# Performance work log

Measured on AMD Instinct MI355X. Metric: run time of the kernel, lower is better.

Reference implementation:

```python
import jax, jax.numpy as jnp
import numpy as np

N_HEAD = 8
N_VIEWS = 26
C = 256
H = W = 32
B_SCENE = 2


def _get_default_angles():
    # Reconstructed: bottom pole, top pole, then 3 rings of 8 azimuths at elev 45/0/-45.
    angs = [(0.0, -90.0), (0.0, 90.0)]
    for phi in (45.0, 0.0, -45.0):
        for k in range(8):
            angs.append((45.0 * k, phi))
    return np.array(angs)


def _angle_select():
    a = _get_default_angles()
    d = np.abs(a.reshape(26, 1, 2) - a.reshape(1, 26, 2))
    d = np.sum(np.minimum(d, 360 - d), axis=2)
    ab = d == 45
    ab[0, -8::2] = True
    ab[-8::2, 0] = True
    ab[1, 2:10:2] = True
    ab[2:10:2, 1] = True
    return [np.argwhere(ab[i]).reshape(-1) for i in range(26)]


def _mha_index(i):
    return i if i < 2 else (i - 2) // 8 + 2


def _mha(q, kv, Wqkv, bqkv, Wo, bo):
    # torch nn.MultiheadAttention, batch_first: packed in_proj, scale = 1/sqrt(head_dim)
    c = q.shape[-1]
    D = c // N_HEAD
    Wq, Wk, Wv = Wqkv[:c], Wqkv[c:2 * c], Wqkv[2 * c:]
    bq, bk, bv = bqkv[:c], bqkv[c:2 * c], bqkv[2 * c:]
    qp = q @ Wq.T + bq
    kp = kv @ Wk.T + bk
    vp = kv @ Wv.T + bv
    B, S, _ = qp.shape
    K = kp.shape[1]
    qh = qp.reshape(B, S, N_HEAD, D).transpose(0, 2, 1, 3)
    kh = kp.reshape(B, K, N_HEAD, D).transpose(0, 2, 1, 3)
    vh = vp.reshape(B, K, N_HEAD, D).transpose(0, 2, 1, 3)
    scores = jnp.einsum('bhqd,bhkd->bhqk', qh, kh) / jnp.sqrt(jnp.asarray(D, qh.dtype))
    att = jax.nn.softmax(scores, axis=-1)
    o = jnp.einsum('bhqk,bhkd->bhqd', att, vh).transpose(0, 2, 1, 3).reshape(B, S, c)
    return o @ Wo.T + bo


def setup_inputs() -> dict:
    key = jax.random.key(0)
    k1, k2, k3 = jax.random.split(key, 3)
    scale = 1.0 / np.sqrt(C)
    return {
        'x': jax.random.normal(k1, (B_SCENE * N_VIEWS, C, H, W), dtype=jnp.float32),
        'w_qkv': jax.random.normal(k2, (5, 3 * C, C), dtype=jnp.float32) * scale,
        'b_qkv': jnp.zeros((5, 3 * C), dtype=jnp.float32),
        'w_out': jax.random.normal(k3, (5, C, C), dtype=jnp.float32) * scale,
        'b_out': jnp.zeros((5, C), dtype=jnp.float32),
    }


def reference(x, w_qkv, b_qkv, w_out, b_out):
    bt, c, h, w = x.shape
    B = bt // N_VIEWS
    # (b t) c h w -> b t (h w) c
    xr = x.reshape(B, N_VIEWS, c, h * w).transpose(0, 1, 3, 2)
    sel = _angle_select()
    outs = []
    for i in range(N_VIEWS):
        m = _mha_index(i)
        q = xr[:, i]                                  # [B, S, c]
        kv = xr[:, sel[i]].reshape(B, -1, c)          # [B, n_nbr*S, c]
        outs.append(_mha(q, kv, w_qkv[m], b_qkv[m], w_out[m], b_out[m]))
    y = jnp.stack(outs, axis=1)                       # b t s c
    return y.transpose(0, 1, 3, 2).reshape(bt, c, h, w)
```

## Files before the change

### kernel.cpp

```cpp
#include <hip/hip_runtime.h>
#include <hip/hip_bf16.h>

#define NV 26
#define NS 1024
#define NC 256
#define NH 8
#define ND 32
#define NPAIR 66

typedef unsigned short u16;
typedef unsigned int u32;
typedef short short8_t __attribute__((ext_vector_type(8)));
typedef float f32x4 __attribute__((ext_vector_type(4)));
typedef unsigned int u32x4 __attribute__((ext_vector_type(4)));

__constant__ int c_view_m[NV]  = {0,1,2,2,2,2,2,2,2,2,3,3,3,3,3,3,3,3,4,4,4,4,4,4,4,4};
__constant__ int c_view_nk[NV] = {4,4,4,3,4,3,4,3,4,3,4,4,4,4,4,4,4,4,4,3,4,3,4,3,4,3};
__constant__ int c_view_kv[NV][4] = {
  {0,1,2,3},      {4,5,6,7},      {8,10,16,17},   {9,11,18,-1},
  {8,10,12,19},   {11,13,20,-1},  {8,12,14,21},   {13,15,22,-1},
  {8,14,16,23},   {9,15,24,-1},   {25,34,40,41},  {26,33,35,42},
  {27,34,36,43},  {28,35,37,44},  {29,36,38,45},  {30,37,39,46},
  {31,38,40,47},  {32,33,39,48},  {49,50,59,65},  {51,58,60,-1},
  {49,52,59,61},  {53,60,62,-1},  {49,54,61,63},  {55,62,64,-1},
  {49,56,63,65},  {57,58,64,-1}
};
__constant__ int c_pair_m[NPAIR] = {
  0,0,0,0, 1,1,1,1,
  2,2,2,2,2,2,2,2,2,2,2,2,2,2,2,2,2,
  3,3,3,3,3,3,3,3,3,3,3,3,3,3,3,3,3,3,3,3,3,3,3,3,
  4,4,4,4,4,4,4,4,4,4,4,4,4,4,4,4,4
};
__constant__ int c_pair_j[NPAIR] = {
  18,20,22,24, 2,4,6,8,
  1,2,3,4,5,6,7,8,9,10,11,12,13,14,15,16,17,
  2,3,4,5,6,7,8,9,10,11,12,13,14,15,16,17,18,19,20,21,22,23,24,25,
  0,10,11,12,13,14,15,16,17,18,19,20,21,22,23,24,25
};

__device__ __forceinline__ float bf16_to_f32(u16 u) {
  return __uint_as_float(((u32)u) << 16);
}
__device__ __forceinline__ u16 f32_to_bf16(float f) {
  u32 u = __float_as_uint(f);
  u32 r = (u + 0x7fffu + ((u >> 16) & 1u)) >> 16;
  return (u16)r;
}
__device__ __forceinline__ float ld_src(const void* p, size_t i, bool isf) {
  return isf ? ((const float*)p)[i] : bf16_to_f32(((const u16*)p)[i]);
}
__device__ __forceinline__ u32 pack_bf16x2_rne(float a, float b) {
  __hip_bfloat162 h = __float22bfloat162_rn(float2{a, b});
  return *(u32*)&h;
}
__device__ __forceinline__ bool detect_isf(const u16* __restrict__ x) {
  float f = fabsf(bf16_to_f32(x[threadIdx.x & 63]));
  if (!(f < 3.0e38f)) f = 3.0e38f;
#pragma unroll
  for (int m = 1; m < 64; m <<= 1) f = fmaxf(f, __shfl_xor(f, m));
  return f > 1.0e6f;
}

#define NW1 983040
#define NW2 327680
#define NB1 3840
#define NB2 1280
__global__ __launch_bounds__(256) void prep_w_kernel(const u16* __restrict__ xdet,
                                                     const void* __restrict__ w_qkv,
                                                     const void* __restrict__ w_out,
                                                     const void* __restrict__ b_qkv,
                                                     const void* __restrict__ b_out,
                                                     u16* __restrict__ Wqkvb, u16* __restrict__ Wob,
                                                     float* __restrict__ bq, float* __restrict__ bo) {
  bool isf = detect_isf(xdet);
  int i = blockIdx.x * 256 + threadIdx.x;
  if (i < NW1) Wqkvb[i] = f32_to_bf16(ld_src(w_qkv, i, isf));
  else if (i < NW1 + NW2) Wob[i - NW1] = f32_to_bf16(ld_src(w_out, i - NW1, isf));
  else if (i < NW1 + NW2 + NB1) bq[i - NW1 - NW2] = ld_src(b_qkv, i - NW1 - NW2, isf);
  else if (i < NW1 + NW2 + NB1 + NB2) bo[i - NW1 - NW2 - NB1] = ld_src(b_out, i - NW1 - NW2 - NB1, isf);
}

__global__ __launch_bounds__(256) void prep_x_kernel(const void* __restrict__ xin,
                                                     u16* __restrict__ Xt) {
  __shared__ float tile[32][33];
  bool isf = detect_isf((const u16*)xin);
  int bt = blockIdx.x;
  int s0 = blockIdx.y * 32, c0 = blockIdx.z * 32;
  int tid = threadIdx.x;
#pragma unroll
  for (int p = 0; p < 4; ++p) {
    int cl = (tid >> 5) + p * 8, sl = tid & 31;
    tile[cl][sl] = ld_src(xin, (size_t)(bt * NC + c0 + cl) * NS + s0 + sl, isf);
  }
  __syncthreads();
  int srow = tid >> 3, c4 = (tid & 7) * 4;
  ushort4 v;
  v.x = f32_to_bf16(tile[c4 + 0][srow]);
  v.y = f32_to_bf16(tile[c4 + 1][srow]);
  v.z = f32_to_bf16(tile[c4 + 2][srow]);
  v.w = f32_to_bf16(tile[c4 + 3][srow]);
  *(ushort4*)&Xt[(size_t)(bt * NS + s0 + srow) * NC + c0 + c4] = v;
}

__device__ __forceinline__ void gemm128(const u16* __restrict__ A, const u16* __restrict__ B,
                                        u16* As, u16* Bs, f32x4 acc[4][4],
                                        int wo, int ws, int lm, int g, int tid) {
#pragma unroll
  for (int i = 0; i < 4; ++i)
#pragma unroll
    for (int j = 0; j < 4; ++j)
#pragma unroll
      for (int r = 0; r < 4; ++r) acc[i][j][r] = 0.f;
  int c0i = tid, c1i = tid + 256;
  const u16* a0p = A + (c0i >> 2) * NC + (c0i & 3) * 8;
  const u16* a1p = A + (c1i >> 2) * NC + (c1i & 3) * 8;
  const u16* b0p = B + (c0i >> 2) * NC + (c0i & 3) * 8;
  const u16* b1p = B + (c1i >> 2) * NC + (c1i & 3) * 8;
  uint4 ra0 = *(const uint4*)(a0p);
  uint4 ra1 = *(const uint4*)(a1p);
  uint4 rb0 = *(const uint4*)(b0p);
  uint4 rb1 = *(const uint4*)(b1p);
  const u16* arow = As + (wo * 64 + lm) * 32 + g * 8;
  const u16* brow = Bs + (ws * 64 + lm) * 32 + g * 8;
#pragma unroll
  for (int k0 = 0; k0 < NC; k0 += 32) {
    __syncthreads();
    *(uint4*)&As[c0i * 8] = ra0;
    *(uint4*)&As[c1i * 8] = ra1;
    *(uint4*)&Bs[c0i * 8] = rb0;
    *(uint4*)&Bs[c1i * 8] = rb1;
    if (k0 + 32 < NC) {
      ra0 = *(const uint4*)(a0p + k0 + 32);
      ra1 = *(const uint4*)(a1p + k0 + 32);
      rb0 = *(const uint4*)(b0p + k0 + 32);
      rb1 = *(const uint4*)(b1p + k0 + 32);
    }
    __syncthreads();
    short8_t af[4], bf[4];
#pragma unroll
    for (int i = 0; i < 4; ++i) af[i] = *(const short8_t*)(arow + i * 16 * 32);
#pragma unroll
    for (int j = 0; j < 4; ++j) bf[j] = *(const short8_t*)(brow + j * 16 * 32);
#pragma unroll
    for (int i = 0; i < 4; ++i)
#pragma unroll
      for (int j = 0; j < 4; ++j)
        acc[i][j] = __builtin_amdgcn_mfma_f32_16x16x32_bf16(af[i], bf[j], acc[i][j], 0, 0, 0);
  }
}

__global__ __launch_bounds__(256, 3) void qkvproj_kernel(const u16* __restrict__ Xt,
                                                         const u16* __restrict__ Wqkvb,
                                                         const float* __restrict__ bq,
                                                         u16* __restrict__ Qb,
                                                         u16* __restrict__ Kb,
                                                         u16* __restrict__ Vb) {
  __shared__ __align__(16) u16 As[128 * 32];
  __shared__ __align__(16) u16 Bs[128 * 32];
  int bid = blockIdx.x;
  int tid = threadIdx.x;
  int wave = tid >> 6, lane = tid & 63, lm = lane & 15, g = lane >> 4;
  int wo = wave >> 1, ws = wave & 1;

  int obase, s0, m, src_bt;
  u16* dst; int dslot; float sc; bool isV = false;
  if (bid < 832) {
    int bt = bid >> 4, rem = bid & 15;
    obase = (rem & 1) * 128; s0 = (rem >> 1) * 128;
    m = c_view_m[bt % NV]; src_bt = bt;
    dst = Qb; dslot = bt; sc = 0.25505653862161186f;
  } else {
    int jb = bid - 832;
    int pb = jb >> 5, rem = jb & 31;
    int ot = rem & 3; s0 = (rem >> 2) * 128;
    obase = 256 + ot * 128;
    m = c_pair_m[pb >> 1]; src_bt = (pb & 1) * NV + c_pair_j[pb >> 1];
    dst = (ot < 2) ? Kb : Vb; dslot = pb; sc = 1.0f;
    isV = (ot >= 2);
  }
  f32x4 acc[4][4];
  gemm128(Wqkvb + (size_t)(m * 768 + obase) * NC,
          Xt + ((size_t)src_bt * NS + s0) * NC, As, Bs, acc, wo, ws, lm, g, tid);
  int osub = (obase < 256) ? 0 : ((obase < 512) ? 256 : 512);
#pragma unroll
  for (int i = 0; i < 4; ++i) {
    int o_r0 = obase + wo * 64 + i * 16 + 4 * g;
    float4 bias = *(const float4*)&bq[m * 768 + o_r0];
    int oloc = o_r0 - osub;
    int h = oloc >> 5, d0 = oloc & 31;
#pragma unroll
    for (int j = 0; j < 4; ++j) {
      int s = s0 + ws * 64 + j * 16 + lm;
      f32x4 c = acc[i][j];
      ushort4 v;
      v.x = f32_to_bf16((c[0] + bias.x) * sc);
      v.y = f32_to_bf16((c[1] + bias.y) * sc);
      v.z = f32_to_bf16((c[2] + bias.z) * sc);
      v.w = f32_to_bf16((c[3] + bias.w) * sc);
      if (isV) {
        u16* vt = dst + ((size_t)(dslot * NH + h) * ND + d0) * NS + s;
        vt[0]      = v.x;
        vt[NS]     = v.y;
        vt[2 * NS] = v.z;
        vt[3 * NS] = v.w;
      } else {
        *(ushort4*)&dst[((size_t)(dslot * NH + h) * NS + s) * ND + d0] = v;
      }
    }
  }
}

__global__ __launch_bounds__(256, 3) void attn_kernel(const u16* __restrict__ Qb,
                                                      const u16* __restrict__ Kb,
                                                      const u16* __restrict__ Vb,
                                                      u16* __restrict__ Ot) {
  int gid = blockIdx.x;
  int grp = (gid >> 5) * 8 + (gid & 7);
  int z = (gid >> 3) & 3;
  int bt = grp >> 3;
  int h = grp & 7;
  int view = bt % NV;
  int b = bt / NV;
  int tid = threadIdx.x;
  int wave = tid >> 6, lane = tid & 63;
  int lm = lane & 15, g = lane >> 4;
  int sbase = z * 256 + wave * 64;
  int nk = c_view_nk[view];

  short8_t qf[4];
  {
    const u16* qrow = Qb + ((size_t)(bt * NH + h) * NS + sbase) * ND;
#pragma unroll
    for (int qt = 0; qt < 4; ++qt)
      qf[qt] = *(const short8_t*)(qrow + (qt * 16 + lm) * ND + g * 8);
  }
  f32x4 accq[4][2];
  f32x4 acc_l[4];
#pragma unroll
  for (int qt = 0; qt < 4; ++qt) {
#pragma unroll
    for (int r = 0; r < 4; ++r) { accq[qt][0][r] = 0.f; accq[qt][1][r] = 0.f; acc_l[qt][r] = 0.f; }
  }
  short8_t ones;
#pragma unroll
  for (int e = 0; e < 8; ++e) ones[e] = (short)0x3F80;

  int tot = nk * 16;

  const int kvo  = lm * ND + g * 8;
  const int vvo0 = lm * NS + g * 8;
  const int vvo1 = (16 + lm) * NS + g * 8;

  auto seg_off = [&](int nn) -> size_t {
    int kvp = c_view_kv[view][nn];
    return (size_t)((kvp * 2 + b) * NH + h) * NS * ND;
  };

  short8_t KA[4], VA[4], KB[4], VB[4];

#define LOADK(DST, KP)                                                        \
  {                                                                           \
    _Pragma("unroll")                                                         \
    for (int kt = 0; kt < 4; ++kt)                                            \
      DST[kt] = *(const short8_t*)((KP) + kt * 16 * ND + kvo);                \
  }
#define LOADV(DST, VP)                                                        \
  {                                                                           \
    DST[0] = *(const short8_t*)((VP) + vvo0);                                 \
    DST[1] = *(const short8_t*)((VP) + vvo0 + 32);                            \
    DST[2] = *(const short8_t*)((VP) + vvo1);                                 \
    DST[3] = *(const short8_t*)((VP) + vvo1 + 32);                            \
  }

  auto compute = [&](const short8_t (&K)[4], const short8_t (&V)[4]) {
    __builtin_amdgcn_s_setprio(1);
#pragma unroll
    for (int qt = 0; qt < 4; ++qt) {
      f32x4 z4 = {0.f, 0.f, 0.f, 0.f};
      f32x4 sv[4];
#pragma unroll
      for (int kt = 0; kt < 4; ++kt)
        sv[kt] = __builtin_amdgcn_mfma_f32_16x16x32_bf16(K[kt], qf[qt], z4, 0, 0, 0);
      u32 w[4][2];
#pragma unroll
      for (int kt = 0; kt < 4; ++kt) {
        float p0 = __builtin_amdgcn_exp2f(sv[kt][0]);
        float p1 = __builtin_amdgcn_exp2f(sv[kt][1]);
        float p2 = __builtin_amdgcn_exp2f(sv[kt][2]);
        float p3 = __builtin_amdgcn_exp2f(sv[kt][3]);
        w[kt][0] = pack_bf16x2_rne(p0, p1);
        w[kt][1] = pack_bf16x2_rne(p2, p3);
      }
      u32 pa[2][4];
#pragma unroll
      for (int kt1 = 0; kt1 < 2; ++kt1) {
#pragma unroll
        for (int hh = 0; hh < 2; ++hh) {
          u32 X = w[2 * kt1][hh], Y = w[2 * kt1 + 1][hh];
          asm("v_permlane32_swap_b32 %0, %1" : "+v"(X), "+v"(Y));
          asm("v_permlane16_swap_b32 %0, %1" : "+v"(X), "+v"(Y));
          pa[kt1][hh] = X;
          pa[kt1][2 + hh] = Y;
        }
      }
      u32x4 a0 = {pa[0][0], pa[0][1], pa[0][2], pa[0][3]};
      u32x4 a1 = {pa[1][0], pa[1][1], pa[1][2], pa[1][3]};
      short8_t pf0 = __builtin_bit_cast(short8_t, a0);
      short8_t pf1 = __builtin_bit_cast(short8_t, a1);
      accq[qt][0] = __builtin_amdgcn_mfma_f32_16x16x32_bf16(pf0, V[0], accq[qt][0], 0, 0, 0);
      accq[qt][0] = __builtin_amdgcn_mfma_f32_16x16x32_bf16(pf1, V[1], accq[qt][0], 0, 0, 0);
      accq[qt][1] = __builtin_amdgcn_mfma_f32_16x16x32_bf16(pf0, V[2], accq[qt][1], 0, 0, 0);
      accq[qt][1] = __builtin_amdgcn_mfma_f32_16x16x32_bf16(pf1, V[3], accq[qt][1], 0, 0, 0);
      acc_l[qt]   = __builtin_amdgcn_mfma_f32_16x16x32_bf16(pf0, ones, acc_l[qt], 0, 0, 0);
      acc_l[qt]   = __builtin_amdgcn_mfma_f32_16x16x32_bf16(pf1, ones, acc_l[qt], 0, 0, 0);
    }
    __builtin_amdgcn_s_setprio(0);
  };

  const u16* kp = Kb + seg_off(0);
  const u16* vp = Vb + seg_off(0);
  LOADK(KA, kp); LOADV(VA, vp);

  for (int cc = 0; cc < tot; cc += 2) {
    const u16 *kp1, *vp1;
    if (((cc + 1) & 15) == 0) {
      size_t o = seg_off((cc + 1) >> 4);
      kp1 = Kb + o; vp1 = Vb + o;
    } else {
      kp1 = kp + 64 * ND; vp1 = vp + 64;
    }
    LOADK(KB, kp1); LOADV(VB, vp1);
    compute(KA, VA);

    const u16 *kp2, *vp2;
    if (((cc + 2) & 15) == 0) {
      if (cc + 2 < tot) { size_t o = seg_off((cc + 2) >> 4); kp2 = Kb + o; vp2 = Vb + o; }
      else { kp2 = kp1; vp2 = vp1; }
    } else {
      kp2 = kp1 + 64 * ND; vp2 = vp1 + 64;
    }
    if (cc + 2 < tot) { LOADK(KA, kp2); LOADV(VA, vp2); }
    compute(KB, VB);
    kp = kp2; vp = vp2;
  }
#undef LOADK
#undef LOADV

#pragma unroll
  for (int qt = 0; qt < 4; ++qt) {
#pragma unroll
    for (int r = 0; r < 4; ++r) {
      float inv = __builtin_amdgcn_rcpf(acc_l[qt][r]);
      int s = sbase + qt * 16 + 4 * g + r;
      u16* op = Ot + (size_t)(bt * NS + s) * NC + h * 32 + lm;
      op[0]  = f32_to_bf16(accq[qt][0][r] * inv);
      op[16] = f32_to_bf16(accq[qt][1][r] * inv);
    }
  }
}

__global__ __launch_bounds__(256, 3) void oproj_kernel(const u16* __restrict__ xdet,
                                                       const u16* __restrict__ Ot,
                                                       const u16* __restrict__ Wob,
                                                       const float* __restrict__ bo,
                                                       void* __restrict__ out) {
  __shared__ __align__(16) u16 As[128 * 32];
  __shared__ __align__(16) u16 Bs[128 * 32];
  bool isf = detect_isf(xdet);
  int bid = blockIdx.x;
  int bt = bid >> 4, rem = bid & 15;
  int obase = (rem & 1) * 128, s0 = (rem >> 1) * 128;
  int m = c_view_m[bt % NV];
  int tid = threadIdx.x;
  int wave = tid >> 6, lane = tid & 63, lm = lane & 15, g = lane >> 4;
  int wo = wave >> 1, ws = wave & 1;
  f32x4 acc[4][4];
  gemm128(Wob + (size_t)(m * NC + obase) * NC,
          Ot + ((size_t)bt * NS + s0) * NC, As, Bs, acc, wo, ws, lm, g, tid);
#pragma unroll
  for (int i = 0; i < 4; ++i) {
    int o_r0 = obase + wo * 64 + i * 16 + 4 * g;
    float4 bias = *(const float4*)&bo[m * NC + o_r0];
#pragma unroll
    for (int j = 0; j < 4; ++j) {
      int s = s0 + ws * 64 + j * 16 + lm;
      f32x4 c = acc[i][j];
      size_t base = (size_t)(bt * NC + o_r0) * NS + s;
      float v0 = c[0] + bias.x, v1 = c[1] + bias.y, v2 = c[2] + bias.z, v3 = c[3] + bias.w;
      if (isf) {
        float* fo = (float*)out;
        fo[base] = v0; fo[base + NS] = v1; fo[base + 2 * NS] = v2; fo[base + 3 * NS] = v3;
      } else {
        u16* ho = (u16*)out;
        ho[base] = f32_to_bf16(v0); ho[base + NS] = f32_to_bf16(v1);
        ho[base + 2 * NS] = f32_to_bf16(v2); ho[base + 3 * NS] = f32_to_bf16(v3);
      }
    }
  }
}


extern "C" void kernel_launch(void* const* d_in, const int* in_sizes, int n_in,
                              void* d_out, int out_size, void* d_ws, size_t ws_size,
                              hipStream_t stream) {
  (void)in_sizes; (void)n_in; (void)out_size;
  const void* x     = d_in[0];
  const void* w_qkv = d_in[1];
  const void* b_qkv = d_in[2];
  const void* w_out = d_in[3];
  const void* b_out = d_in[4];

  if (ws_size < 222842880ull) return;

  char* wsb = (char*)d_ws;
  float* bq    = (float*)(wsb + 0);
  float* bo    = (float*)(wsb + 15360);
  u16*   Wqkvb = (u16*)(wsb + 20480);
  u16*   Wob   = (u16*)(wsb + 1986560);
  u16*   Xt    = (u16*)(wsb + 2641920);
  u16*   Qb    = (u16*)(wsb + 29904896);
  u16*   Kb    = (u16*)(wsb + 57167872);
  u16*   Vb    = (u16*)(wsb + 126373888);
  u16*   Ot    = (u16*)(wsb + 195579904);

  prep_w_kernel<<<5140, 256, 0, stream>>>((const u16*)x, w_qkv, w_out, b_qkv, b_out,
                                          Wqkvb, Wob, bq, bo);
  prep_x_kernel<<<dim3(52, 32, 8), 256, 0, stream>>>(x, Xt);
  qkvproj_kernel<<<5056, 256, 0, stream>>>(Xt, Wqkvb, bq, Qb, Kb, Vb);
  attn_kernel<<<1664, 256, 0, stream>>>(Qb, Kb, Vb, Ot);
  oproj_kernel<<<832, 256, 0, stream>>>((const u16*)x, Ot, Wob, bo, d_out);
}
```

Baseline: 585.3 us.

## Drop register double-buffering in attention loop, raise occupancy, use hardware bf16 pack

Removes the manual two-stage K/V register prefetch in the attention kernel and replaces it with a simple per-chunk load-then-compute loop. This frees VGPRs, so launch bounds are raised to allow 4 blocks per CU instead of 3, letting wave-level parallelism hide memory latency instead of explicit prefetch. The softmax probability packing now uses the v_cvt_pk_bf16_f32 instruction instead of the library RNE conversion. The risk is exposed load latency within each wave if the extra occupancy does not cover it.

```diff
diff --git a/kernel.cpp b/kernel.cpp
--- a/kernel.cpp
+++ b/kernel.cpp
@@ -49,6 +49,11 @@
 __device__ __forceinline__ float ld_src(const void* p, size_t i, bool isf) {
   return isf ? ((const float*)p)[i] : bf16_to_f32(((const u16*)p)[i]);
 }
+__device__ __forceinline__ u32 cvt_pk_bf16(float a, float b) {
+  u32 r;
+  asm("v_cvt_pk_bf16_f32 %0, %1, %2" : "=v"(r) : "v"(a), "v"(b));
+  return r;
+}
 __device__ __forceinline__ u32 pack_bf16x2_rne(float a, float b) {
   __hip_bfloat162 h = __float22bfloat162_rn(float2{a, b});
   return *(u32*)&h;
@@ -210,7 +215,7 @@
   }
 }
 
-__global__ __launch_bounds__(256, 3) void attn_kernel(const u16* __restrict__ Qb,
+__global__ __launch_bounds__(256, 4) void attn_kernel(const u16* __restrict__ Qb,
                                                       const u16* __restrict__ Kb,
                                                       const u16* __restrict__ Vb,
                                                       u16* __restrict__ Ot) {
@@ -256,23 +261,19 @@
     return (size_t)((kvp * 2 + b) * NH + h) * NS * ND;
   };
 
-  short8_t KA[4], VA[4], KB[4], VB[4];
-
-#define LOADK(DST, KP)                                                        \
-  {                                                                           \
-    _Pragma("unroll")                                                         \
-    for (int kt = 0; kt < 4; ++kt)                                            \
-      DST[kt] = *(const short8_t*)((KP) + kt * 16 * ND + kvo);                \
-  }
-#define LOADV(DST, VP)                                                        \
-  {                                                                           \
-    DST[0] = *(const short8_t*)((VP) + vvo0);                                 \
-    DST[1] = *(const short8_t*)((VP) + vvo0 + 32);                            \
-    DST[2] = *(const short8_t*)((VP) + vvo1);                                 \
-    DST[3] = *(const short8_t*)((VP) + vvo1 + 32);                            \
-  }
-
-  auto compute = [&](const short8_t (&K)[4], const short8_t (&V)[4]) {
+  const u16* kp = Kb + seg_off(0);
+  const u16* vp = Vb + seg_off(0);
+
+  for (int cc = 0; cc < tot; ++cc) {
+    short8_t K[4], V[4];
+#pragma unroll
+    for (int kt = 0; kt < 4; ++kt)
+      K[kt] = *(const short8_t*)(kp + kt * 16 * ND + kvo);
+    V[0] = *(const short8_t*)(vp + vvo0);
+    V[1] = *(const short8_t*)(vp + vvo0 + 32);
+    V[2] = *(const short8_t*)(vp + vvo1);
+    V[3] = *(const short8_t*)(vp + vvo1 + 32);
+
     __builtin_amdgcn_s_setprio(1);
 #pragma unroll
     for (int qt = 0; qt < 4; ++qt) {
@@ -288,8 +289,8 @@
         float p1 = __builtin_amdgcn_exp2f(sv[kt][1]);
         float p2 = __builtin_amdgcn_exp2f(sv[kt][2]);
         float p3 = __builtin_amdgcn_exp2f(sv[kt][3]);
-        w[kt][0] = pack_bf16x2_rne(p0, p1);
-        w[kt][1] = pack_bf16x2_rne(p2, p3);
+        w[kt][0] = cvt_pk_bf16(p0, p1);
+        w[kt][1] = cvt_pk_bf16(p2, p3);
       }
       u32 pa[2][4];
 #pragma unroll
@@ -315,36 +316,13 @@
       acc_l[qt]   = __builtin_amdgcn_mfma_f32_16x16x32_bf16(pf1, ones, acc_l[qt], 0, 0, 0);
     }
     __builtin_amdgcn_s_setprio(0);
-  };
-
-  const u16* kp = Kb + seg_off(0);
-  const u16* vp = Vb + seg_off(0);
-  LOADK(KA, kp); LOADV(VA, vp);
-
-  for (int cc = 0; cc < tot; cc += 2) {
-    const u16 *kp1, *vp1;
+
     if (((cc + 1) & 15) == 0) {
-      size_t o = seg_off((cc + 1) >> 4);
-      kp1 = Kb + o; vp1 = Vb + o;
+      if (cc + 1 < tot) { size_t o = seg_off((cc + 1) >> 4); kp = Kb + o; vp = Vb + o; }
     } else {
-      kp1 = kp + 64 * ND; vp1 = vp + 64;
-    }
-    LOADK(KB, kp1); LOADV(VB, vp1);
-    compute(KA, VA);
-
-    const u16 *kp2, *vp2;
-    if (((cc + 2) & 15) == 0) {
-      if (cc + 2 < tot) { size_t o = seg_off((cc + 2) >> 4); kp2 = Kb + o; vp2 = Vb + o; }
-      else { kp2 = kp1; vp2 = vp1; }
-    } else {
-      kp2 = kp1 + 64 * ND; vp2 = vp1 + 64;
-    }
-    if (cc + 2 < tot) { LOADK(KA, kp2); LOADV(VA, vp2); }
-    compute(KB, VB);
-    kp = kp2; vp = vp2;
-  }
-#undef LOADK
-#undef LOADV
+      kp += 64 * ND; vp += 64;
+    }
+  }
 
 #pragma unroll
   for (int qt = 0; qt < 4; ++qt) {
```

After: 550.7 us. 1.06x faster.
